# Kernel tuning notes

Measured on AMD Instinct MI355X. Metric: run time of the kernel, lower is better.

Reference implementation:

```python
import jax, jax.numpy as jnp
import numpy as np
from jax import lax

C = 128        # args.feat_dim
HF = WF = 320  # feature map spatial size
IMG = 1280     # segmentation map resolution
N = 256        # number of anchors
CROP = 32      # fixed crop size (h and w)
NUM_CLASSES = 151
NUM_BASE = 64


def setup_inputs() -> dict:
    key = jax.random.key(0)
    ks = jax.random.split(key, 9)
    feature_map = jax.random.normal(ks[0], (C, HF, WF), dtype=jnp.float32)
    seg = jax.random.randint(ks[1], (IMG, IMG), 0, NUM_CLASSES, dtype=jnp.int32)
    x0 = jax.random.randint(ks[2], (N,), 0, WF - CROP, dtype=jnp.int32)
    y0 = jax.random.randint(ks[3], (N,), 0, HF - CROP, dtype=jnp.int32)
    # anchors layout matches torch code: [x0, x1, y0, y1] in feature-map pixels
    anchors = jnp.stack([x0, x0 + CROP, y0, y0 + CROP], axis=1)
    labels = jax.random.randint(ks[4], (N,), 0, NUM_BASE, dtype=jnp.int32)
    base_classes = jax.random.randint(ks[5], (NUM_BASE,), 0, NUM_CLASSES, dtype=jnp.int32)
    W1 = jax.random.normal(ks[6], (256, C, 3, 3), dtype=jnp.float32) * 0.02
    b1 = jnp.zeros((256,), dtype=jnp.float32)
    W2 = jax.random.normal(ks[7], (1, 256, 3, 3), dtype=jnp.float32) * 0.02
    b2 = jnp.zeros((1,), dtype=jnp.float32)
    return {"feature_map": feature_map, "seg": seg, "anchors": anchors,
            "labels": labels, "base_classes": base_classes,
            "W1": W1, "b1": b1, "W2": W2, "b2": b2}


def reference(feature_map, seg, anchors, labels, base_classes, W1, b1, W2, b2):
    # F.interpolate(mode='nearest') from IMGxIMG down to HFxWF: idx = floor(i * in/out)
    hi = (jnp.arange(HF) * seg.shape[0]) // HF
    wi = (jnp.arange(WF) * seg.shape[1]) // WF
    mask = seg[hi][:, wi].astype(jnp.float32)  # [HF, WF]

    starts = anchors[:, jnp.array([2, 0])]  # (h0, w0) per anchor

    def crop_feat(s):
        return lax.dynamic_slice(feature_map, (jnp.int32(0), s[0], s[1]), (C, CROP, CROP))

    def crop_mask(s):
        return lax.dynamic_slice(mask, (s[0], s[1]), (CROP, CROP))

    crops = jax.vmap(crop_feat)(starts)       # [N, C, CROP, CROP]
    mask_crops = jax.vmap(crop_mask)(starts)  # [N, CROP, CROP]

    dn = ('NCHW', 'OIHW', 'NCHW')
    h = lax.conv_general_dilated(crops, W1, (1, 1), 'SAME', dimension_numbers=dn)
    h = jax.nn.relu(h + b1[None, :, None, None])
    logits = lax.conv_general_dilated(h, W2, (1, 1), 'SAME', dimension_numbers=dn)
    logits = logits + b2[None, :, None, None]  # [N, 1, CROP, CROP]

    tgt_cls = base_classes[labels].astype(jnp.float32)  # [N]
    tgt = (mask_crops == tgt_cls[:, None, None]).astype(jnp.float32)[:, None]  # [N,1,CROP,CROP]

    # stable BCE-with-logits: max(x,0) - x*t + log1p(exp(-|x|))
    bce = jnp.maximum(logits, 0.0) - logits * tgt + jnp.log1p(jnp.exp(-jnp.abs(logits)))
    per_anchor = bce.mean(axis=(1, 2, 3))  # mean per anchor, as in F.binary_cross_entropy_with_logits
    return per_anchor.sum() / (N + 1e-10)
```

## Files before the change

kernel.cpp:

```cpp
#include <hip/hip_runtime.h>

typedef __attribute__((ext_vector_type(8))) short short8;
typedef __attribute__((ext_vector_type(8))) int int8v;
typedef __attribute__((ext_vector_type(16))) float floatx16;
typedef __attribute__((ext_vector_type(4))) unsigned int uint4v;
typedef unsigned short ushort_t;
typedef unsigned int uint_t;
typedef unsigned char uchar_t;

#define NA   256
#define CIN  128
#define HFD  320
#define FMPX (HFD*HFD)
#define IMGD 1280

#define W1R_BYTE_OFF (1u<<20)
#define W2R_BYTE_OFF ((1u<<20) + 9*256*128)
#define FMT_BYTE_OFF (2u<<20)

#define SAPL_Q 5440
#define PSTR_Q 4112

union V32 { int8v v; uint4v q[2]; };

__device__ __forceinline__ ushort_t f2bf(float v) {
    uint_t u = __float_as_uint(v);
    return (ushort_t)((u + 0x8000u) >> 16);
}
__device__ __forceinline__ uchar_t f2fp8(float v) {
    int r = __builtin_amdgcn_cvt_pk_fp8_f32(v, 0.0f, 0, false);
    return (uchar_t)(r & 0xff);
}

__global__ __launch_bounds__(256) void prep_misc(
    const float* __restrict__ W1, const float* __restrict__ W2,
    float* __restrict__ logits, float* __restrict__ out,
    uchar_t* __restrict__ w1b, ushort_t* __restrict__ w2r)
{
    const int b = blockIdx.x, t = threadIdx.x;
    if (b < 1024) {
        logits[b * 256 + t] = 0.0f;
    } else if (b < 1024 + 128) {
        int e = (b - 1024) * 256 + t;
        int oc = e >> 7, cin = e & 127;
        int g = oc >> 6, nt = (oc >> 5) & 1, lv = oc & 31;
        int c = cin >> 6, kh = (cin >> 5) & 1, j = cin & 31;
        #pragma unroll
        for (int tap = 0; tap < 9; ++tap) {
            int idx = (((((tap * 4 + g) * 2 + nt) * 2 + c) * 64) + kh * 32 + lv) * 32 + j;
            w1b[idx] = f2fp8(W1[(oc * 128 + cin) * 9 + tap] * 64.0f);
        }
    } else {
        #pragma unroll
        for (int i = 0; i < 32; ++i) {
            int e = i * 256 + t;
            int nrow = e >> 8, oc = e & 255;
            w2r[nrow * 256 + oc] = f2bf(nrow < 9 ? W2[oc * 9 + nrow] : 0.0f);
        }
        if (t == 0) out[0] = 0.0f;
    }
}

__global__ __launch_bounds__(256) void prep_transpose(
    const float* __restrict__ fm, uchar_t* __restrict__ fmT)
{
    __shared__ uchar_t s[32 * 144];
    const int t = threadIdx.x;
    const int y = blockIdx.y, x0b = blockIdx.x * 32;
    #pragma unroll
    for (int i = 0; i < 16; ++i) {
        int e = t + 256 * i;
        int c = e >> 5, xo = e & 31;
        s[xo * 144 + c] = f2fp8(fm[(size_t)c * FMPX + y * HFD + x0b + xo]);
    }
    __syncthreads();
    {
        int xo = t >> 3, cg = t & 7;
        uint4v v = *(const uint4v*)&s[xo * 144 + cg * 16];
        *(uint4v*)&fmT[((size_t)(y * HFD + x0b + xo)) * 128 + cg * 16] = v;
    }
}

__global__ __launch_bounds__(256, 3) void conv_mfma_kernel(
    const int* __restrict__ anchors, const uchar_t* __restrict__ fmT,
    const uchar_t* __restrict__ w1b, const ushort_t* __restrict__ w2r,
    const float* __restrict__ b1, float* __restrict__ logits)
{
    const int id   = blockIdx.x;
    const int xcd  = id & 7, sid = id >> 3;
    const int n    = xcd * 32 + (sid >> 4);
    const int rem  = sid & 15;
    const int q    = rem >> 2;
    const int g    = rem & 3;

    const int t    = threadIdx.x;
    const int w    = t >> 6;
    const int lane = t & 63;
    const int l31  = lane & 31;
    const int kh   = lane >> 5;

    const int x0 = anchors[n * 4 + 0];
    const int y0 = anchors[n * 4 + 2];
    const int r0 = q * 8;

    __shared__ __align__(16) char smem[8 * PSTR_Q];
    char* s_a = smem;

    if (t < 80) {
        int sub = t & 3, k = t >> 2;
        int pr = k >> 1, col = (k & 1) * 33;
        uint4v z = {0u, 0u, 0u, 0u};
        *(uint4v*)(s_a + sub * SAPL_Q + (pr * 34 + col) * 16) = z;
    }

    floatx16 acc[2][2];
    #pragma unroll
    for (int mt = 0; mt < 2; ++mt)
        #pragma unroll
        for (int nt = 0; nt < 2; ++nt)
            #pragma unroll
            for (int r = 0; r < 16; ++r) acc[mt][nt][r] = 0.0f;

    auto loadB = [&](int tap, int cc, V32* b) {
        #pragma unroll
        for (int nt = 0; nt < 2; ++nt) {
            const uchar_t* bp = w1b + ((((tap * 4 + g) * 2 + nt) * 2 + cc) << 11) + lane * 32;
            b[nt].q[0] = *(const uint4v*)(bp);
            b[nt].q[1] = *(const uint4v*)(bp + 16);
        }
    };

#define MF4(AL, AH, BB)                                                                   \
    acc[0][0] = __builtin_amdgcn_mfma_scale_f32_32x32x64_f8f6f4(                          \
        (AL).v, (BB)[0].v, acc[0][0], 0, 0, 0, 127, 0, 127);                              \
    acc[0][1] = __builtin_amdgcn_mfma_scale_f32_32x32x64_f8f6f4(                          \
        (AL).v, (BB)[1].v, acc[0][1], 0, 0, 0, 127, 0, 127);                              \
    acc[1][0] = __builtin_amdgcn_mfma_scale_f32_32x32x64_f8f6f4(                          \
        (AH).v, (BB)[0].v, acc[1][0], 0, 0, 0, 127, 0, 127);                              \
    acc[1][1] = __builtin_amdgcn_mfma_scale_f32_32x32x64_f8f6f4(                          \
        (AH).v, (BB)[1].v, acc[1][1], 0, 0, 0, 127, 0, 127);

    V32 bb0[2], bb1[2], bb2[2];
    loadB(0, 0, bb0);
    loadB(3, 0, bb1);

    #pragma unroll 1
    for (int c = 0; c < 2; ++c) {
        __syncthreads();
        #pragma unroll
        for (int j = 0; j < 5; ++j) {
            int u = t + 256 * j;
            int pr = u >> 7, rr = u & 127;
            int cell = rr >> 2, sub = rr & 3;
            int cr = r0 + pr - 1;
            uint4v v = {0u, 0u, 0u, 0u};
            if ((unsigned)cr < 32u)
                v = *(const uint4v*)&fmT[((size_t)((y0 + cr) * HFD + x0 + cell)) * 128 + c * 64 + sub * 16];
            *(uint4v*)(s_a + sub * SAPL_Q + (pr * 34 + cell + 1) * 16) = v;
        }
        __syncthreads();

        #pragma unroll 1
        for (int gi = 0; gi < 3; ++gi) {
            V32 fa0, fa1, fa2, fa3;
            {
                const char* ap = s_a + (2 * kh) * SAPL_Q + ((2 * w) * 34 + l31 + gi) * 16;
                fa0.q[0] = *(const uint4v*)(ap);
                fa0.q[1] = *(const uint4v*)(ap + SAPL_Q);
                fa1.q[0] = *(const uint4v*)(ap + 544);
                fa1.q[1] = *(const uint4v*)(ap + SAPL_Q + 544);
                fa2.q[0] = *(const uint4v*)(ap + 1088);
                fa2.q[1] = *(const uint4v*)(ap + SAPL_Q + 1088);
                fa3.q[0] = *(const uint4v*)(ap + 1632);
                fa3.q[1] = *(const uint4v*)(ap + SAPL_Q + 1632);
            }
            const int last = (gi == 2);
            const int tapk1 = last ? 0 : gi + 1;
            const int tapk2 = last ? 3 : gi + 4;
            const int ccn   = last ? 1 : c;

            loadB(6 + gi, c, bb2);
            MF4(fa0, fa1, bb0)
            loadB(tapk1, ccn, bb0);
            MF4(fa1, fa2, bb1)
            loadB(tapk2, ccn, bb1);
            MF4(fa2, fa3, bb2)
        }
    }
#undef MF4

    __syncthreads();
    #pragma unroll
    for (int nt = 0; nt < 2; ++nt) {
        float bias = b1[g * 64 + nt * 32 + l31];
        int plane = nt * 4 + (l31 >> 3);
        #pragma unroll
        for (int mt = 0; mt < 2; ++mt) {
            int lr = 2 * w + mt;
            #pragma unroll
            for (int reg = 0; reg < 16; ++reg) {
                int col = (reg & 3) + 8 * (reg >> 2) + 4 * kh;
                float hv = fmaxf(fmaf(acc[mt][nt][reg], 0.015625f, bias), 0.0f);
                *(ushort_t*)(smem + plane * PSTR_Q + ((lr * 32 + col) * 8 + (l31 & 7)) * 2) = f2bf(hv);
            }
        }
    }
    __syncthreads();

    floatx16 vacc[2];
    #pragma unroll
    for (int mt = 0; mt < 2; ++mt)
        #pragma unroll
        for (int r = 0; r < 16; ++r) vacc[mt][r] = 0.0f;
    #pragma unroll
    for (int ks = 0; ks < 4; ++ks) {
        short8 bw = *(const short8*)&w2r[l31 * 256 + g * 64 + ks * 16 + kh * 8];
        #pragma unroll
        for (int mt = 0; mt < 2; ++mt) {
            short8 ah = *(const short8*)(smem + (ks * 2 + kh) * PSTR_Q + ((2 * w + mt) * 32 + l31) * 16);
            vacc[mt] = __builtin_amdgcn_mfma_f32_32x32x16_bf16(ah, bw, vacc[mt], 0, 0, 0);
        }
    }

    __syncthreads();
    float* s_log = (float*)smem;
    for (int i = t; i < 320; i += 256) s_log[i] = 0.0f;
    __syncthreads();
    if (l31 < 9) {
        int ky = l31 / 3, kx = l31 - ky * 3;
        #pragma unroll
        for (int mt = 0; mt < 2; ++mt) {
            int outr = 2 * w + mt + 2 - ky;
            #pragma unroll
            for (int reg = 0; reg < 16; ++reg) {
                int col  = (reg & 3) + 8 * (reg >> 2) + 4 * kh;
                int outc = col + 1 - kx;
                if (outc >= 0 && outc < 32)
                    atomicAdd(&s_log[outr * 32 + outc], vacc[mt][reg]);
            }
        }
    }
    __syncthreads();
    for (int i = t; i < 320; i += 256) {
        int outr = i >> 5, outc = i & 31;
        int R = r0 + outr - 1;
        if ((unsigned)R < 32u)
            atomicAdd(&logits[n * 1024 + R * 32 + outc], s_log[i]);
    }
}

__global__ __launch_bounds__(256) void bce_reduce_kernel(
    const float* __restrict__ logits, const int* __restrict__ seg,
    const int* __restrict__ anchors, const int* __restrict__ labels,
    const int* __restrict__ base_classes, const float* __restrict__ b2,
    float* __restrict__ out)
{
    const int n = blockIdx.x;
    const int t = threadIdx.x;
    const int y0 = anchors[n * 4 + 2];
    const int x0 = anchors[n * 4 + 0];
    const int tgt_cls = base_classes[labels[n]];
    const float bias2 = b2[0];

    float lsum = 0.0f;
    #pragma unroll
    for (int r = 0; r < 4; ++r) {
        int p = t + r * 256;
        int i = p >> 5, j = p & 31;
        float l = logits[n * 1024 + p] + bias2;
        int sv = seg[(size_t)(4 * (y0 + i)) * IMGD + 4 * (x0 + j)];
        float tgt = (sv == tgt_cls) ? 1.0f : 0.0f;
        lsum += fmaxf(l, 0.0f) - l * tgt + log1pf(expf(-fabsf(l)));
    }
    #pragma unroll
    for (int off = 32; off > 0; off >>= 1) lsum += __shfl_down(lsum, off, 64);
    __shared__ float s[4];
    if ((t & 63) == 0) s[t >> 6] = lsum;
    __syncthreads();
    if (t == 0) {
        float tot = s[0] + s[1] + s[2] + s[3];
        const float scale = 1.0f / (1024.0f * (256.0f + 1e-10f));
        atomicAdd(out, tot * scale);
    }
}

extern "C" void kernel_launch(void* const* d_in, const int* in_sizes, int n_in,
                              void* d_out, int out_size, void* d_ws, size_t ws_size,
                              hipStream_t stream) {
    const float* fm           = (const float*)d_in[0];
    const int*   seg          = (const int*)d_in[1];
    const int*   anchors      = (const int*)d_in[2];
    const int*   labels       = (const int*)d_in[3];
    const int*   base_classes = (const int*)d_in[4];
    const float* W1           = (const float*)d_in[5];
    const float* b1           = (const float*)d_in[6];
    const float* W2           = (const float*)d_in[7];
    const float* b2           = (const float*)d_in[8];
    float* out = (float*)d_out;

    float*    logits = (float*)d_ws;
    uchar_t*  w1b    = (uchar_t*)((char*)d_ws + W1R_BYTE_OFF);
    ushort_t* w2r    = (ushort_t*)((char*)d_ws + W2R_BYTE_OFF);
    uchar_t*  fmT    = (uchar_t*)((char*)d_ws + FMT_BYTE_OFF);

    prep_misc<<<1024 + 128 + 1, 256, 0, stream>>>(W1, W2, logits, out, w1b, w2r);
    prep_transpose<<<dim3(10, 320), 256, 0, stream>>>(fm, fmT);
    conv_mfma_kernel<<<4096, 256, 0, stream>>>(anchors, fmT, w1b, w2r, b1, logits);
    bce_reduce_kernel<<<NA, 256, 0, stream>>>(logits, seg, anchors, labels, base_classes, b2, out);
}
```

Baseline: 226.6 us.

## Merge prep kernels and fuse BCE reduction into conv via last-block counter

Combines the feature-map transpose and the weight/zero prep into one launch, and removes the separate BCE kernel. Each anchor's 16 conv blocks now bump a per-anchor counter, and the last one to finish computes that anchor's BCE and adds it to the output. This cuts launch count from four to two and drops the tail gaps between kernels. In exchange it adds threadfences and atomics at the end of every conv block. It also changes the transpose's shared-memory row pitch from 144 to 176.

```diff
diff --git a/kernel.cpp b/kernel.cpp
--- a/kernel.cpp
+++ b/kernel.cpp
@@ -16,6 +16,7 @@
 
 #define W1R_BYTE_OFF (1u<<20)
 #define W2R_BYTE_OFF ((1u<<20) + 9*256*128)
+#define CNT_BYTE_OFF (1536u<<10)
 #define FMT_BYTE_OFF (2u<<20)
 
 #define SAPL_Q 5440
@@ -32,16 +33,31 @@
     return (uchar_t)(r & 0xff);
 }
 
-__global__ __launch_bounds__(256) void prep_misc(
+__global__ __launch_bounds__(256) void prep_kernel(
     const float* __restrict__ W1, const float* __restrict__ W2,
+    const float* __restrict__ fm,
     float* __restrict__ logits, float* __restrict__ out,
-    uchar_t* __restrict__ w1b, ushort_t* __restrict__ w2r)
+    uchar_t* __restrict__ w1b, ushort_t* __restrict__ w2r,
+    uchar_t* __restrict__ fmT, uint_t* __restrict__ cnt)
 {
     const int b = blockIdx.x, t = threadIdx.x;
-    if (b < 1024) {
-        logits[b * 256 + t] = 0.0f;
-    } else if (b < 1024 + 128) {
-        int e = (b - 1024) * 256 + t;
+    __shared__ uchar_t s[32 * 176];
+    if (b < 3200) {
+        const int y = b / 10, x0b = (b % 10) * 32;
+        #pragma unroll
+        for (int i = 0; i < 16; ++i) {
+            int e = t + 256 * i;
+            int c = e >> 5, xo = e & 31;
+            s[xo * 176 + c] = f2fp8(fm[(size_t)c * FMPX + y * HFD + x0b + xo]);
+        }
+        __syncthreads();
+        int xo = t >> 3, cg = t & 7;
+        uint4v v = *(const uint4v*)&s[xo * 176 + cg * 16];
+        *(uint4v*)&fmT[((size_t)(y * HFD + x0b + xo)) * 128 + cg * 16] = v;
+    } else if (b < 4224) {
+        logits[(b - 3200) * 256 + t] = 0.0f;
+    } else if (b < 4352) {
+        int e = (b - 4224) * 256 + t;
         int oc = e >> 7, cin = e & 127;
         int g = oc >> 6, nt = (oc >> 5) & 1, lv = oc & 31;
         int c = cin >> 6, kh = (cin >> 5) & 1, j = cin & 31;
@@ -57,34 +73,18 @@
             int nrow = e >> 8, oc = e & 255;
             w2r[nrow * 256 + oc] = f2bf(nrow < 9 ? W2[oc * 9 + nrow] : 0.0f);
         }
+        cnt[t] = 0u;
         if (t == 0) out[0] = 0.0f;
-    }
-}
-
-__global__ __launch_bounds__(256) void prep_transpose(
-    const float* __restrict__ fm, uchar_t* __restrict__ fmT)
-{
-    __shared__ uchar_t s[32 * 144];
-    const int t = threadIdx.x;
-    const int y = blockIdx.y, x0b = blockIdx.x * 32;
-    #pragma unroll
-    for (int i = 0; i < 16; ++i) {
-        int e = t + 256 * i;
-        int c = e >> 5, xo = e & 31;
-        s[xo * 144 + c] = f2fp8(fm[(size_t)c * FMPX + y * HFD + x0b + xo]);
-    }
-    __syncthreads();
-    {
-        int xo = t >> 3, cg = t & 7;
-        uint4v v = *(const uint4v*)&s[xo * 144 + cg * 16];
-        *(uint4v*)&fmT[((size_t)(y * HFD + x0b + xo)) * 128 + cg * 16] = v;
     }
 }
 
 __global__ __launch_bounds__(256, 3) void conv_mfma_kernel(
     const int* __restrict__ anchors, const uchar_t* __restrict__ fmT,
     const uchar_t* __restrict__ w1b, const ushort_t* __restrict__ w2r,
-    const float* __restrict__ b1, float* __restrict__ logits)
+    const float* __restrict__ b1, float* __restrict__ logits,
+    const int* __restrict__ seg, const int* __restrict__ labels,
+    const int* __restrict__ base_classes, const float* __restrict__ b2,
+    float* __restrict__ out, uint_t* __restrict__ cnt)
 {
     const int id   = blockIdx.x;
     const int xcd  = id & 7, sid = id >> 3;
@@ -104,6 +104,7 @@
     const int r0 = q * 8;
 
     __shared__ __align__(16) char smem[8 * PSTR_Q];
+    __shared__ int s_done;
     char* s_a = smem;
 
     if (t < 80) {
@@ -247,40 +248,39 @@
         if ((unsigned)R < 32u)
             atomicAdd(&logits[n * 1024 + R * 32 + outc], s_log[i]);
     }
-}
-
-__global__ __launch_bounds__(256) void bce_reduce_kernel(
-    const float* __restrict__ logits, const int* __restrict__ seg,
-    const int* __restrict__ anchors, const int* __restrict__ labels,
-    const int* __restrict__ base_classes, const float* __restrict__ b2,
-    float* __restrict__ out)
-{
-    const int n = blockIdx.x;
-    const int t = threadIdx.x;
-    const int y0 = anchors[n * 4 + 2];
-    const int x0 = anchors[n * 4 + 0];
-    const int tgt_cls = base_classes[labels[n]];
-    const float bias2 = b2[0];
-
-    float lsum = 0.0f;
-    #pragma unroll
-    for (int r = 0; r < 4; ++r) {
-        int p = t + r * 256;
-        int i = p >> 5, j = p & 31;
-        float l = logits[n * 1024 + p] + bias2;
-        int sv = seg[(size_t)(4 * (y0 + i)) * IMGD + 4 * (x0 + j)];
-        float tgt = (sv == tgt_cls) ? 1.0f : 0.0f;
-        lsum += fmaxf(l, 0.0f) - l * tgt + log1pf(expf(-fabsf(l)));
-    }
-    #pragma unroll
-    for (int off = 32; off > 0; off >>= 1) lsum += __shfl_down(lsum, off, 64);
-    __shared__ float s[4];
-    if ((t & 63) == 0) s[t >> 6] = lsum;
+
+    __threadfence();
     __syncthreads();
     if (t == 0) {
-        float tot = s[0] + s[1] + s[2] + s[3];
-        const float scale = 1.0f / (1024.0f * (256.0f + 1e-10f));
-        atomicAdd(out, tot * scale);
+        uint_t old = atomicAdd(&cnt[n], 1u);
+        s_done = (old == 15u) ? 1 : 0;
+    }
+    __syncthreads();
+    if (s_done) {
+        __threadfence();
+        const int tgt_cls = base_classes[labels[n]];
+        const float bias2 = b2[0];
+        float lsum = 0.0f;
+        #pragma unroll
+        for (int r = 0; r < 4; ++r) {
+            int p = t + r * 256;
+            int i = p >> 5, j = p & 31;
+            float l = __hip_atomic_load(&logits[n * 1024 + p],
+                                        __ATOMIC_RELAXED, __HIP_MEMORY_SCOPE_AGENT) + bias2;
+            int sv = seg[(size_t)(4 * (y0 + i)) * IMGD + 4 * (x0 + j)];
+            float tgt = (sv == tgt_cls) ? 1.0f : 0.0f;
+            lsum += fmaxf(l, 0.0f) - l * tgt + log1pf(expf(-fabsf(l)));
+        }
+        #pragma unroll
+        for (int off = 32; off > 0; off >>= 1) lsum += __shfl_down(lsum, off, 64);
+        float* s_red = (float*)smem;
+        if ((t & 63) == 0) s_red[t >> 6] = lsum;
+        __syncthreads();
+        if (t == 0) {
+            float tot = s_red[0] + s_red[1] + s_red[2] + s_red[3];
+            const float scale = 1.0f / (1024.0f * (256.0f + 1e-10f));
+            atomicAdd(out, tot * scale);
+        }
     }
 }
 
@@ -301,10 +301,10 @@
     float*    logits = (float*)d_ws;
     uchar_t*  w1b    = (uchar_t*)((char*)d_ws + W1R_BYTE_OFF);
     ushort_t* w2r    = (ushort_t*)((char*)d_ws + W2R_BYTE_OFF);
+    uint_t*   cnt    = (uint_t*)((char*)d_ws + CNT_BYTE_OFF);
     uchar_t*  fmT    = (uchar_t*)((char*)d_ws + FMT_BYTE_OFF);
 
-    prep_misc<<<1024 + 128 + 1, 256, 0, stream>>>(W1, W2, logits, out, w1b, w2r);
-    prep_transpose<<<dim3(10, 320), 256, 0, stream>>>(fm, fmT);
-    conv_mfma_kernel<<<4096, 256, 0, stream>>>(anchors, fmT, w1b, w2r, b1, logits);
-    bce_reduce_kernel<<<NA, 256, 0, stream>>>(logits, seg, anchors, labels, base_classes, b2, out);
-}
+    prep_kernel<<<4353, 256, 0, stream>>>(W1, W2, fm, logits, out, w1b, w2r, fmT, cnt);
+    conv_mfma_kernel<<<4096, 256, 0, stream>>>(anchors, fmT, w1b, w2r, b1, logits,
+                                               seg, labels, base_classes, b2, out, cnt);
+}
```

After: 467.3 us. 106% more time.
